# Kernel optimization log

Measured on AMD Instinct MI355X. Metric: run time of the kernel, lower is better.

The kernel has to match this reference:

```python
import jax, jax.numpy as jnp
import numpy as np

C = 768      # token feature dim
N = 196      # tokens per stream
R_DIM = 2 * 2 * N  # 784 = concat(A row, A col)


def setup_inputs() -> dict:
    key = jax.random.key(0)
    ks = jax.random.split(key, 16)
    s = 1.0 / np.sqrt(C)
    inp = {
        "x": jax.random.normal(ks[0], (128, N, C), dtype=jnp.float32),
        "y": jax.random.normal(ks[1], (128, N, C), dtype=jnp.float32),
        # linear_conv_1: 1x1 conv (768->768) + BN affine (eval) + ReLU
        "W1": jax.random.normal(ks[2], (C, C), dtype=jnp.float32) * s,
        "b1": jnp.zeros((C,), dtype=jnp.float32),
        "g1": jax.random.uniform(ks[3], (C,), dtype=jnp.float32, minval=0.5, maxval=1.5),
        "be1": jax.random.normal(ks[4], (C,), dtype=jnp.float32) * 0.1,
        # linear_conv_2
        "W2": jax.random.normal(ks[5], (C, C), dtype=jnp.float32) * s,
        "b2": jnp.zeros((C,), dtype=jnp.float32),
        "g2": jax.random.uniform(ks[6], (C,), dtype=jnp.float32, minval=0.5, maxval=1.5),
        "be2": jax.random.normal(ks[7], (C,), dtype=jnp.float32) * 0.1,
        # linear_conv_3: 768->768
        "W3": jax.random.normal(ks[8], (C, C), dtype=jnp.float32) * s,
        "b3": jnp.zeros((C,), dtype=jnp.float32),
        # linear_conv_4: 784->784 over relation rows
        "W4": jax.random.normal(ks[9], (784, 784), dtype=jnp.float32) / np.sqrt(784.0),
        "b4": jnp.zeros((784,), dtype=jnp.float32),
        # linear_conv_5: (768+784)->1
        "W5": jax.random.normal(ks[10], (C + 784, 1), dtype=jnp.float32) / np.sqrt(C + 784.0),
        "b5": jnp.zeros((1,), dtype=jnp.float32),
    }
    return inp


def reference(x, y, W1, b1, g1, be1, W2, b2, g2, be2, W3, b3, W4, b4, W5, b5):
    # per-token 1x1 conv + BN(eval)->affine + ReLU
    phi_x = jax.nn.relu((x @ W1 + b1) * g1 + be1)          # [B,196,768]
    phi_y = jax.nn.relu((y @ W2 + b2) * g2 + be2)          # [B,196,768]
    cat_phi = jnp.concatenate([phi_x, phi_y], axis=1)      # [B,392,768]
    # affinity matrix A = cat_phi @ cat_phi^T
    A = jnp.einsum("bnd,bmd->bnm", cat_phi, cat_phi)       # [B,392,392]
    # R[i] = concat(A[i,:], A[:,i]) -> vectorized as [A | A^T]
    R = jnp.concatenate([A, jnp.swapaxes(A, 1, 2)], axis=2)  # [B,392,784]
    v = cat_phi @ W3 + b3                                   # [B,392,768]
    v_ = R @ W4 + b4                                        # [B,392,784]
    cat_v = jnp.concatenate([v, v_], axis=2)                # [B,392,1552]
    W = cat_v @ W5 + b5                                     # [B,392,1]
    # per-token reweighting then sum of the two streams
    out = x * W[:, :N, :] + y * W[:, N:, :]                 # [B,196,768]
    return out
```

## Files before the change

kernel.cpp:

```cpp
#include <hip/hip_runtime.h>

typedef __bf16 bf16_t;
typedef bf16_t bf16x8 __attribute__((ext_vector_type(8)));
typedef float f32x4 __attribute__((ext_vector_type(4)));
typedef unsigned short u16x8 __attribute__((ext_vector_type(8)));
typedef unsigned short u16x4 __attribute__((ext_vector_type(4)));

#define CD 768
#define NT 196
#define NB 128
#define T2 392
#define MROWS (NB*NT)
#define NTILE 1176

__device__ __forceinline__ unsigned short f2bf(float f){
  unsigned u = __float_as_uint(f);
  u += 0x7fffu + ((u >> 16) & 1u);
  return (unsigned short)(u >> 16);
}
__device__ __forceinline__ float bf2f(unsigned short h){
  return __uint_as_float(((unsigned)h) << 16);
}
__device__ __forceinline__ float wave_reduce(float v){
  #pragma unroll
  for (int o = 32; o > 0; o >>= 1) v += __shfl_down(v, o, 64);
  return v;
}
__device__ __forceinline__ void gload16(const unsigned short* g, unsigned short* l){
  __builtin_amdgcn_global_load_lds(
      (const __attribute__((address_space(1))) unsigned int*)g,
      (__attribute__((address_space(3))) unsigned int*)l, 16, 0, 0);
}

__global__ __launch_bounds__(256) void prep_wt(const float* __restrict__ W1,
                        const float* __restrict__ W2,
                        unsigned short* __restrict__ W1t, unsigned short* __restrict__ W2t){
  __shared__ float tile[64][65];
  const float* src = blockIdx.z ? W2 : W1;
  unsigned short* dst = blockIdx.z ? W2t : W1t;
  int k0 = blockIdx.x*64, n0 = blockIdx.y*64;
  int tid = threadIdx.x;
  #pragma unroll
  for (int e = 0; e < 16; ++e){
    int idx = e*256 + tid;
    int r = idx >> 6, c = idx & 63;
    tile[r][c] = src[(size_t)(k0+r)*CD + n0 + c];
  }
  __syncthreads();
  #pragma unroll
  for (int e = 0; e < 16; ++e){
    int idx = e*256 + tid;
    int nr = idx >> 6, kc = idx & 63;
    dst[(size_t)(n0+nr)*CD + k0 + kc] = f2bf(tile[kc][nr]);
  }
}

__global__ void prep_u(const float* __restrict__ W3, const float* __restrict__ W4,
                       const float* __restrict__ W5, const float* __restrict__ b3,
                       const float* __restrict__ b4, const float* __restrict__ b5,
                       float* __restrict__ u3, float* __restrict__ u4s, float* __restrict__ cbuf){
  int wid = (blockIdx.x*blockDim.x + threadIdx.x) >> 6;
  int lane = threadIdx.x & 63;
  const float* w5a = W5;
  const float* w5b = W5 + CD;
  float s = 0.f;
  if (wid < CD){
    const float* row = W3 + (size_t)wid*CD;
    for (int k = lane; k < CD; k += 64) s += row[k]*w5a[k];
    s = wave_reduce(s);
    if (lane == 0) u3[wid] = s;
  } else if (wid < CD + T2){
    int j = wid - CD;
    const float* r0 = W4 + (size_t)j*784;
    const float* r1 = W4 + (size_t)(j+T2)*784;
    for (int e = lane; e < 784; e += 64) s += (r0[e]+r1[e])*w5b[e];
    s = wave_reduce(s);
    if (lane == 0) u4s[j] = s;
  } else if (wid == CD + T2){
    for (int k = lane; k < CD; k += 64) s += b3[k]*w5a[k];
    for (int e = lane; e < 784; e += 64) s += b4[e]*w5b[e];
    s = wave_reduce(s);
    if (lane == 0) cbuf[0] = s + b5[0];
  }
}

__global__ void init_t(const float* __restrict__ u3, float* __restrict__ t){
  int i = blockIdx.x*256 + threadIdx.x;
  if (i < (NB+1)*CD) t[i] = (i < NB*CD) ? u3[i % CD] : 0.f;
}

__global__ __launch_bounds__(256) void cvt2(const float* __restrict__ x,
                                            const float* __restrict__ y,
                                            unsigned short* __restrict__ dst){
  const int nv = MROWS*CD/8;
  for (int id = blockIdx.x*256 + threadIdx.x; id < 2*nv; id += gridDim.x*256){
    const float* s = (id < nv) ? x : y;
    int i = (id < nv) ? id : id - nv;
    float4 a = ((const float4*)s)[i*2];
    float4 b = ((const float4*)s)[i*2+1];
    u16x8 o = { f2bf(a.x), f2bf(a.y), f2bf(a.z), f2bf(a.w),
                f2bf(b.x), f2bf(b.y), f2bf(b.z), f2bf(b.w) };
    ((u16x8*)dst)[id] = o;
  }
}

__global__ __launch_bounds__(256, 4) void phi_gemm2(
    const unsigned short* __restrict__ Ax, const unsigned short* __restrict__ Ay,
    const unsigned short* __restrict__ Bx, const unsigned short* __restrict__ By,
    const float* __restrict__ biasX, const float* __restrict__ gamX, const float* __restrict__ betX,
    const float* __restrict__ biasY, const float* __restrict__ gamY, const float* __restrict__ betY,
    const float* __restrict__ u4s,
    unsigned short* __restrict__ Px, unsigned short* __restrict__ Py,
    float* __restrict__ t, int mode)
{
  __shared__ unsigned short As[128*64];
  __shared__ unsigned short Bs[128*64];

  const int tid  = threadIdx.x;
  const int lane = tid & 63;
  const int w    = tid >> 6;
  const int wr = w >> 1, wc = w & 1;

  const int chunk = gridDim.x >> 3;
  int orig = blockIdx.x;
  int swz  = (orig & 7)*chunk + (orig >> 3);
  int s, r;
  if (mode < 0){ s = swz >= NTILE; r = swz - s*NTILE; }
  else         { s = mode; r = swz; }
  const int bn = r % 6;
  const int bm = r / 6;

  const unsigned short* A   = s ? Ay : Ax;
  const unsigned short* Bt  = s ? By : Bx;
  const float* bias = s ? biasY : biasX;
  const float* gam  = s ? gamY  : gamX;
  const float* bet  = s ? betY  : betX;
  const float* u4c  = u4s + s*NT;
  unsigned short* phi = s ? Py : Px;

  const int srow = lane >> 3;
  const int p    = lane & 7;
  const int g0   = (p - srow) & 7;
  const unsigned short* a0 = A  + (size_t)(bm*128 + w*32 + srow)*CD + g0*8;
  const unsigned short* b0 = Bt + (size_t)(bn*128 + w*32 + srow)*CD + g0*8;
  unsigned short* al = &As[(w*32)*64];
  unsigned short* bl = &Bs[(w*32)*64];

  const int fr = lane & 15, f = lane >> 4, r7 = lane & 7;
  f32x4 acc[4][4] = {};

  #pragma unroll 1
  for (int kt = 0; kt < 12; ++kt){
    const int ko = kt*64;
    #pragma unroll
    for (int c = 0; c < 4; ++c){
      gload16(a0 + (size_t)c*8*CD + ko, al + c*512);
      gload16(b0 + (size_t)c*8*CD + ko, bl + c*512);
    }
    __syncthreads();
    #pragma unroll
    for (int kk = 0; kk < 2; ++kk){
      bf16x8 af[4], bq[4];
      #pragma unroll
      for (int mi = 0; mi < 4; ++mi){ int rr = wr*64 + mi*16 + fr;
        af[mi] = *(const bf16x8*)(&As[rr*64 + (((kk*4+f)+r7)&7)*8]); }
      #pragma unroll
      for (int ni = 0; ni < 4; ++ni){ int cc = wc*64 + ni*16 + fr;
        bq[ni] = *(const bf16x8*)(&Bs[cc*64 + (((kk*4+f)+r7)&7)*8]); }
      #pragma unroll
      for (int mi = 0; mi < 4; ++mi)
        #pragma unroll
        for (int ni = 0; ni < 4; ++ni)
          acc[mi][ni] = __builtin_amdgcn_mfma_f32_16x16x32_bf16(af[mi], bq[ni], acc[mi][ni], 0, 0, 0);
    }
    if (kt < 11) __syncthreads();
  }

  const int b_base = (bm*128) / NT;
  #pragma unroll
  for (int ni = 0; ni < 4; ++ni){
    int col = bn*128 + wc*64 + ni*16 + fr;
    float bi = bias[col], ga = gam[col], be = bet[col];
    float c0 = 0.f, c1 = 0.f;
    #pragma unroll
    for (int mi = 0; mi < 4; ++mi){
      int r0 = bm*128 + wr*64 + mi*16 + f*4;
      #pragma unroll
      for (int j = 0; j < 4; ++j){
        int rr = r0 + j;
        float v = fmaxf((acc[mi][ni][j] + bi)*ga + be, 0.f);
        phi[(size_t)rr*CD + col] = f2bf(v);
        int b = rr / NT;
        int tok = rr - b*NT;
        float pv = u4c[tok]*v;
        if (b == b_base) c0 += pv; else c1 += pv;
      }
    }
    c0 += __shfl_xor(c0, 16, 64); c0 += __shfl_xor(c0, 32, 64);
    c1 += __shfl_xor(c1, 16, 64); c1 += __shfl_xor(c1, 32, 64);
    if (lane < 16){
      atomicAdd(&t[(size_t)b_base*CD + col], c0);
      atomicAdd(&t[(size_t)(b_base+1)*CD + col], c1);
    }
  }
}

template<bool USEBF>
__global__ __launch_bounds__(256) void comp_wout(
    const unsigned short* __restrict__ phiX, const unsigned short* __restrict__ phiY,
    const float* __restrict__ t, const float* __restrict__ cbuf,
    const float* __restrict__ x, const float* __restrict__ y,
    const unsigned short* __restrict__ xb, const unsigned short* __restrict__ yb,
    float* __restrict__ out)
{
  int gw   = (blockIdx.x*256 + threadIdx.x) >> 6;
  int lane = threadIdx.x & 63;
  int b = gw / NT;
  const unsigned short* px = phiX + (size_t)gw*CD;
  const unsigned short* py = phiY + (size_t)gw*CD;
  const float* tb = t + (size_t)b*CD;
  float s1 = 0.f, s2 = 0.f;
  #pragma unroll
  for (int it = 0; it < 3; ++it){
    int k = it*256 + lane*4;
    float4 tv = *(const float4*)(tb + k);
    u16x4 ux = *(const u16x4*)(px + k);
    u16x4 uy = *(const u16x4*)(py + k);
    s1 += bf2f(ux.x)*tv.x + bf2f(ux.y)*tv.y + bf2f(ux.z)*tv.z + bf2f(ux.w)*tv.w;
    s2 += bf2f(uy.x)*tv.x + bf2f(uy.y)*tv.y + bf2f(uy.z)*tv.z + bf2f(uy.w)*tv.w;
  }
  s1 = wave_reduce(s1);
  s2 = wave_reduce(s2);
  float cc = cbuf[0];
  float wx = __shfl(s1, 0, 64) + cc;
  float wy = __shfl(s2, 0, 64) + cc;
  float* orow = out + (size_t)gw*CD;
  #pragma unroll
  for (int it = 0; it < 3; ++it){
    int k = it*256 + lane*4;
    float4 xv, yv;
    if (USEBF){
      u16x4 a  = *(const u16x4*)(xb + (size_t)gw*CD + k);
      u16x4 c4 = *(const u16x4*)(yb + (size_t)gw*CD + k);
      xv = float4{bf2f(a.x), bf2f(a.y), bf2f(a.z), bf2f(a.w)};
      yv = float4{bf2f(c4.x), bf2f(c4.y), bf2f(c4.z), bf2f(c4.w)};
    } else {
      xv = *(const float4*)(x + (size_t)gw*CD + k);
      yv = *(const float4*)(y + (size_t)gw*CD + k);
    }
    float4 o;
    o.x = xv.x*wx + yv.x*wy;
    o.y = xv.y*wx + yv.y*wy;
    o.z = xv.z*wx + yv.z*wy;
    o.w = xv.w*wx + yv.w*wy;
    *(float4*)(orow + k) = o;
  }
}

extern "C" void kernel_launch(void* const* d_in, const int* in_sizes, int n_in,
                              void* d_out, int out_size, void* d_ws, size_t ws_size,
                              hipStream_t stream){
  const float* x  = (const float*)d_in[0];
  const float* y  = (const float*)d_in[1];
  const float* W1 = (const float*)d_in[2];
  const float* b1 = (const float*)d_in[3];
  const float* g1 = (const float*)d_in[4];
  const float* be1= (const float*)d_in[5];
  const float* W2 = (const float*)d_in[6];
  const float* b2 = (const float*)d_in[7];
  const float* g2 = (const float*)d_in[8];
  const float* be2= (const float*)d_in[9];
  const float* W3 = (const float*)d_in[10];
  const float* b3 = (const float*)d_in[11];
  const float* W4 = (const float*)d_in[12];
  const float* b4 = (const float*)d_in[13];
  const float* W5 = (const float*)d_in[14];
  const float* b5 = (const float*)d_in[15];
  float* out = (float*)d_out;

  const size_t BIGE = (size_t)MROWS*CD;
  const size_t smallF = CD + T2 + 4 + (size_t)(NB+1)*CD;
  const size_t need4 = (2*(size_t)CD*CD + 4*BIGE)*2 + smallF*4 + 256;
  const bool big = (ws_size >= need4);

  unsigned short* W1t = (unsigned short*)d_ws;
  unsigned short* W2t = W1t + CD*CD;
  unsigned short* Sx  = W2t + CD*CD;
  unsigned short* Sy  = Sx + BIGE;
  unsigned short* Px, * Py;
  float* smalls;
  if (big){
    Px = Sy + BIGE;
    Py = Px + BIGE;
    smalls = (float*)(Py + BIGE);
  } else {
    Px = Sy + BIGE;
    Py = Sx;
    smalls = (float*)(Px + BIGE);
  }
  float* u3   = smalls;
  float* u4s  = u3 + CD;
  float* cbuf = u4s + T2;
  float* t    = cbuf + 4;

  prep_wt<<<dim3(12,12,2), 256, 0, stream>>>(W1, W2, W1t, W2t);
  prep_u<<<(CD + T2 + 4)/4, 256, 0, stream>>>(W3, W4, W5, b3, b4, b5, u3, u4s, cbuf);
  init_t<<<((NB+1)*CD + 255)/256, 256, 0, stream>>>(u3, t);

  cvt2<<<2048, 256, 0, stream>>>(x, y, Sx);

  if (big){
    phi_gemm2<<<2*NTILE, 256, 0, stream>>>(Sx, Sy, W1t, W2t,
        b1, g1, be1, b2, g2, be2, u4s, Px, Py, t, -1);
    comp_wout<true><<<MROWS/4, 256, 0, stream>>>(Px, Py, t, cbuf, x, y, Sx, Sy, out);
  } else {
    phi_gemm2<<<NTILE, 256, 0, stream>>>(Sx, Sy, W1t, W2t,
        b1, g1, be1, b2, g2, be2, u4s, Px, Py, t, 0);
    phi_gemm2<<<NTILE, 256, 0, stream>>>(Sx, Sy, W1t, W2t,
        b1, g1, be1, b2, g2, be2, u4s, Px, Py, t, 1);
    comp_wout<false><<<MROWS/4, 256, 0, stream>>>(Px, Py, t, cbuf, x, y, Sx, Sy, out);
  }
}
```

Baseline: 199.1 us.

## Enlarge phi GEMM tiles to 256x256 with double-buffered LDS and 8 waves

```diff
diff --git a/kernel.cpp b/kernel.cpp
--- a/kernel.cpp
+++ b/kernel.cpp
@@ -11,7 +11,11 @@
 #define NB 128
 #define T2 392
 #define MROWS (NB*NT)
-#define NTILE 1176
+#define BM 256
+#define BN 256
+#define NMT 98
+#define NNT 3
+#define TILES (NMT*NNT)
 
 __device__ __forceinline__ unsigned short f2bf(float f){
   unsigned u = __float_as_uint(f);
@@ -86,7 +90,7 @@
 
 __global__ void init_t(const float* __restrict__ u3, float* __restrict__ t){
   int i = blockIdx.x*256 + threadIdx.x;
-  if (i < (NB+1)*CD) t[i] = (i < NB*CD) ? u3[i % CD] : 0.f;
+  if (i < (NB+2)*CD) t[i] = (i < NB*CD) ? u3[i % CD] : 0.f;
 }
 
 __global__ __launch_bounds__(256) void cvt2(const float* __restrict__ x,
@@ -104,7 +108,7 @@
   }
 }
 
-__global__ __launch_bounds__(256, 4) void phi_gemm2(
+__global__ __launch_bounds__(512, 2) void phi_gemm2(
     const unsigned short* __restrict__ Ax, const unsigned short* __restrict__ Ay,
     const unsigned short* __restrict__ Bx, const unsigned short* __restrict__ By,
     const float* __restrict__ biasX, const float* __restrict__ gamX, const float* __restrict__ betX,
@@ -113,22 +117,25 @@
     unsigned short* __restrict__ Px, unsigned short* __restrict__ Py,
     float* __restrict__ t, int mode)
 {
-  __shared__ unsigned short As[128*64];
-  __shared__ unsigned short Bs[128*64];
+  __shared__ unsigned short As[2][BM*64];
+  __shared__ unsigned short Bs[2][BN*64];
 
   const int tid  = threadIdx.x;
   const int lane = tid & 63;
   const int w    = tid >> 6;
-  const int wr = w >> 1, wc = w & 1;
-
-  const int chunk = gridDim.x >> 3;
-  int orig = blockIdx.x;
-  int swz  = (orig & 7)*chunk + (orig >> 3);
-  int s, r;
-  if (mode < 0){ s = swz >= NTILE; r = swz - s*NTILE; }
-  else         { s = mode; r = swz; }
-  const int bn = r % 6;
-  const int bm = r / 6;
+  const int wm = w >> 2, wn = w & 3;
+
+  const int nw = gridDim.x;
+  const int q8 = nw >> 3, r8 = nw & 7;
+  const int xcd = blockIdx.x & 7;
+  const int tt  = blockIdx.x >> 3;
+  int swz = (xcd < r8 ? xcd*(q8+1) : r8*(q8+1) + (xcd-r8)*q8) + tt;
+
+  int s, rr;
+  if (mode < 0){ s = swz >= TILES; rr = swz - s*TILES; }
+  else         { s = mode; rr = swz; }
+  const int bn = rr % NNT;
+  const int bm = rr / NNT;
 
   const unsigned short* A   = s ? Ay : Ax;
   const unsigned short* Bt  = s ? By : Bx;
@@ -138,69 +145,108 @@
   const float* u4c  = u4s + s*NT;
   unsigned short* phi = s ? Py : Px;
 
-  const int srow = lane >> 3;
-  const int p    = lane & 7;
-  const int g0   = (p - srow) & 7;
-  const unsigned short* a0 = A  + (size_t)(bm*128 + w*32 + srow)*CD + g0*8;
-  const unsigned short* b0 = Bt + (size_t)(bn*128 + w*32 + srow)*CD + g0*8;
-  unsigned short* al = &As[(w*32)*64];
-  unsigned short* bl = &Bs[(w*32)*64];
-
-  const int fr = lane & 15, f = lane >> 4, r7 = lane & 7;
-  f32x4 acc[4][4] = {};
+  const int g0 = ((tid & 7) - (tid >> 3)) & 7;
+  const unsigned short* aB = A  + (size_t)(bm*BM + (tid>>3))*CD + g0*8;
+  const unsigned short* bB = Bt + (size_t)(bn*BN + (tid>>3))*CD + g0*8;
+
+  const int fr = lane & 15, f = lane >> 4;
+  const int ph0 = (f     + (fr & 7)) & 7;
+  const int ph1 = (4 + f + (fr & 7)) & 7;
+
+  f32x4 acc[8][4];
+  #pragma unroll
+  for (int mi = 0; mi < 8; ++mi)
+    #pragma unroll
+    for (int ni = 0; ni < 4; ++ni) acc[mi][ni] = f32x4{0.f,0.f,0.f,0.f};
+
+#define STAGE(D, KT) { const int ko = (KT)*64;                         \
+    _Pragma("unroll")                                                  \
+    for (int cc = 0; cc < 4; ++cc){                                    \
+      gload16(aB + (size_t)cc*64*CD + ko, &As[D][cc*4096 + tid*8]);    \
+      gload16(bB + (size_t)cc*64*CD + ko, &Bs[D][cc*4096 + tid*8]); } }
+
+#define RD_B(KK) {                                                     \
+    _Pragma("unroll")                                                  \
+    for (int ni = 0; ni < 4; ++ni)                                     \
+      bq[ni] = *(const bf16x8*)(&cB[(wn*64 + ni*16 + fr)*64 + ((KK)?ph1:ph0)*8]); }
+
+#define RD_A(MH, KK) {                                                 \
+    _Pragma("unroll")                                                  \
+    for (int m2 = 0; m2 < 4; ++m2)                                     \
+      af[m2] = *(const bf16x8*)(&cA[(wm*128 + (MH)*64 + m2*16 + fr)*64 + ((KK)?ph1:ph0)*8]); }
+
+#define MMA(MH) {                                                      \
+    _Pragma("unroll")                                                  \
+    for (int m2 = 0; m2 < 4; ++m2)                                     \
+      _Pragma("unroll")                                                \
+      for (int ni = 0; ni < 4; ++ni)                                   \
+        acc[(MH)*4+m2][ni] = __builtin_amdgcn_mfma_f32_16x16x32_bf16(af[m2], bq[ni], acc[(MH)*4+m2][ni], 0, 0, 0); }
+
+  STAGE(0, 0)
+  asm volatile("s_waitcnt vmcnt(0)" ::: "memory");
+  __builtin_amdgcn_s_barrier();
 
   #pragma unroll 1
   for (int kt = 0; kt < 12; ++kt){
-    const int ko = kt*64;
+    const int D = kt & 1;
+    const unsigned short* cA = As[D];
+    const unsigned short* cB = Bs[D];
+    bf16x8 af[4], bq[4];
+
+    if (kt < 11) STAGE(D^1, kt+1)
+    RD_B(0) RD_A(0, 0)
+    __builtin_amdgcn_s_barrier();
+    __builtin_amdgcn_s_setprio(1); MMA(0) __builtin_amdgcn_s_setprio(0);
+    __builtin_amdgcn_s_barrier();
+    RD_A(1, 0)
+    __builtin_amdgcn_s_barrier();
+    __builtin_amdgcn_s_setprio(1); MMA(1) __builtin_amdgcn_s_setprio(0);
+    __builtin_amdgcn_s_barrier();
+    RD_B(1) RD_A(0, 1)
+    __builtin_amdgcn_s_barrier();
+    __builtin_amdgcn_s_setprio(1); MMA(0) __builtin_amdgcn_s_setprio(0);
+    __builtin_amdgcn_s_barrier();
+    RD_A(1, 1)
+    __builtin_amdgcn_s_barrier();
+    __builtin_amdgcn_s_setprio(1); MMA(1) __builtin_amdgcn_s_setprio(0);
+    asm volatile("s_waitcnt vmcnt(0)" ::: "memory");
+    __builtin_amdgcn_s_barrier();
+  }
+#undef MMA
+#undef RD_A
+#undef RD_B
+#undef STAGE
+
+  const int b_base = (bm*BM) / NT;
+  #pragma unroll
+  for (int ni = 0; ni < 4; ++ni){
+    int col = bn*BN + wn*64 + ni*16 + fr;
+    float bi = bias[col], ga = gam[col], be = bet[col];
+    float cb0 = 0.f, cb1 = 0.f, cb2 = 0.f;
     #pragma unroll
-    for (int c = 0; c < 4; ++c){
-      gload16(a0 + (size_t)c*8*CD + ko, al + c*512);
-      gload16(b0 + (size_t)c*8*CD + ko, bl + c*512);
-    }
-    __syncthreads();
-    #pragma unroll
-    for (int kk = 0; kk < 2; ++kk){
-      bf16x8 af[4], bq[4];
-      #pragma unroll
-      for (int mi = 0; mi < 4; ++mi){ int rr = wr*64 + mi*16 + fr;
-        af[mi] = *(const bf16x8*)(&As[rr*64 + (((kk*4+f)+r7)&7)*8]); }
-      #pragma unroll
-      for (int ni = 0; ni < 4; ++ni){ int cc = wc*64 + ni*16 + fr;
-        bq[ni] = *(const bf16x8*)(&Bs[cc*64 + (((kk*4+f)+r7)&7)*8]); }
-      #pragma unroll
-      for (int mi = 0; mi < 4; ++mi)
-        #pragma unroll
-        for (int ni = 0; ni < 4; ++ni)
-          acc[mi][ni] = __builtin_amdgcn_mfma_f32_16x16x32_bf16(af[mi], bq[ni], acc[mi][ni], 0, 0, 0);
-    }
-    if (kt < 11) __syncthreads();
-  }
-
-  const int b_base = (bm*128) / NT;
-  #pragma unroll
-  for (int ni = 0; ni < 4; ++ni){
-    int col = bn*128 + wc*64 + ni*16 + fr;
-    float bi = bias[col], ga = gam[col], be = bet[col];
-    float c0 = 0.f, c1 = 0.f;
-    #pragma unroll
-    for (int mi = 0; mi < 4; ++mi){
-      int r0 = bm*128 + wr*64 + mi*16 + f*4;
+    for (int mi = 0; mi < 8; ++mi){
+      int r0 = bm*BM + wm*128 + mi*16 + f*4;
       #pragma unroll
       for (int j = 0; j < 4; ++j){
-        int rr = r0 + j;
+        int rg = r0 + j;
         float v = fmaxf((acc[mi][ni][j] + bi)*ga + be, 0.f);
-        phi[(size_t)rr*CD + col] = f2bf(v);
-        int b = rr / NT;
-        int tok = rr - b*NT;
+        phi[(size_t)rg*CD + col] = f2bf(v);
+        int b = rg / NT;
+        int tok = rg - b*NT;
         float pv = u4c[tok]*v;
-        if (b == b_base) c0 += pv; else c1 += pv;
+        int bk = b - b_base;
+        cb0 += (bk == 0) ? pv : 0.f;
+        cb1 += (bk == 1) ? pv : 0.f;
+        cb2 += (bk == 2) ? pv : 0.f;
       }
     }
-    c0 += __shfl_xor(c0, 16, 64); c0 += __shfl_xor(c0, 32, 64);
-    c1 += __shfl_xor(c1, 16, 64); c1 += __shfl_xor(c1, 32, 64);
+    cb0 += __shfl_xor(cb0, 16, 64); cb0 += __shfl_xor(cb0, 32, 64);
+    cb1 += __shfl_xor(cb1, 16, 64); cb1 += __shfl_xor(cb1, 32, 64);
+    cb2 += __shfl_xor(cb2, 16, 64); cb2 += __shfl_xor(cb2, 32, 64);
     if (lane < 16){
-      atomicAdd(&t[(size_t)b_base*CD + col], c0);
-      atomicAdd(&t[(size_t)(b_base+1)*CD + col], c1);
+      atomicAdd(&t[(size_t)(b_base  )*CD + col], cb0);
+      atomicAdd(&t[(size_t)(b_base+1)*CD + col], cb1);
+      atomicAdd(&t[(size_t)(b_base+2)*CD + col], cb2);
     }
   }
 }
@@ -279,7 +325,7 @@
   float* out = (float*)d_out;
 
   const size_t BIGE = (size_t)MROWS*CD;
-  const size_t smallF = CD + T2 + 4 + (size_t)(NB+1)*CD;
+  const size_t smallF = CD + T2 + 4 + (size_t)(NB+2)*CD;
   const size_t need4 = (2*(size_t)CD*CD + 4*BIGE)*2 + smallF*4 + 256;
   const bool big = (ws_size >= need4);
 
@@ -305,18 +351,18 @@
 
   prep_wt<<<dim3(12,12,2), 256, 0, stream>>>(W1, W2, W1t, W2t);
   prep_u<<<(CD + T2 + 4)/4, 256, 0, stream>>>(W3, W4, W5, b3, b4, b5, u3, u4s, cbuf);
-  init_t<<<((NB+1)*CD + 255)/256, 256, 0, stream>>>(u3, t);
+  init_t<<<((NB+2)*CD + 255)/256, 256, 0, stream>>>(u3, t);
 
   cvt2<<<2048, 256, 0, stream>>>(x, y, Sx);
 
   if (big){
-    phi_gemm2<<<2*NTILE, 256, 0, stream>>>(Sx, Sy, W1t, W2t,
+    phi_gemm2<<<2*TILES, 512, 0, stream>>>(Sx, Sy, W1t, W2t,
         b1, g1, be1, b2, g2, be2, u4s, Px, Py, t, -1);
     comp_wout<true><<<MROWS/4, 256, 0, stream>>>(Px, Py, t, cbuf, x, y, Sx, Sy, out);
   } else {
-    phi_gemm2<<<NTILE, 256, 0, stream>>>(Sx, Sy, W1t, W2t,
+    phi_gemm2<<<TILES, 512, 0, stream>>>(Sx, Sy, W1t, W2t,
         b1, g1, be1, b2, g2, be2, u4s, Px, Py, t, 0);
-    phi_gemm2<<<NTILE, 256, 0, stream>>>(Sx, Sy, W1t, W2t,
+    phi_gemm2<<<TILES, 512, 0, stream>>>(Sx, Sy, W1t, W2t,
         b1, g1, be1, b2, g2, be2, u4s, Px, Py, t, 1);
     comp_wout<false><<<MROWS/4, 256, 0, stream>>>(Px, Py, t, cbuf, x, y, Sx, Sy, out);
   }
```

Measured after the change: 250.9 us. 1.26x slower.
